# Kernel optimization log

Hardware: AMD Instinct MI355X
Metric: run time of the kernel (lower is better)

Reference implementation:

```python
import jax, jax.numpy as jnp
import numpy as np

D_MODEL, D_HID, N_EXPERTS, TOP_K = 1024, 4096, 8, 2

def setup_inputs() -> dict:
    key = jax.random.key(0)
    ks = jax.random.split(key, 6)
    B, T = 2, 2048
    x = jax.random.normal(ks[0], (B, T, D_MODEL), dtype=jnp.float32)
    gate_w = jax.random.normal(ks[1], (N_EXPERTS, D_MODEL), dtype=jnp.float32) * (1.0 / np.sqrt(D_MODEL))
    # kaiming_uniform-ish init for expert weights
    lim1 = np.sqrt(6.0 / D_MODEL)
    lim2 = np.sqrt(6.0 / D_HID)
    w1 = jax.random.uniform(ks[2], (N_EXPERTS, D_MODEL, D_HID), dtype=jnp.float32, minval=-lim1, maxval=lim1)
    w2 = jax.random.uniform(ks[3], (N_EXPERTS, D_HID, D_MODEL), dtype=jnp.float32, minval=-lim2, maxval=lim2)
    b1 = jnp.zeros((N_EXPERTS, 1, D_HID), dtype=jnp.float32)
    b2 = jnp.zeros((N_EXPERTS, 1, D_MODEL), dtype=jnp.float32)
    return {"x": x, "gate_w": gate_w, "w1": w1, "b1": b1, "w2": w2, "b2": b2}

def reference(x, gate_w, w1, b1, w2, b2):
    B, T, D = x.shape
    E = gate_w.shape[0]
    xf = x.reshape(-1, D)                              # [N, D]
    N = xf.shape[0]
    # Router: logits -> softmax -> top-k -> renormalize
    logits = jnp.einsum('nd,ed->ne', xf, gate_w)       # [N, E]
    scores = jax.nn.softmax(logits, axis=-1)
    top_w, top_i = jax.lax.top_k(scores, TOP_K)        # [N, K]
    top_w = top_w / jnp.sum(top_w, axis=-1, keepdims=True)
    # Dense combine weights (zero for unselected experts) — same math as
    # the padded-bmm dispatch/combine: padded slots have weight 0.
    gates = jnp.zeros((N, E), xf.dtype).at[jnp.arange(N)[:, None], top_i].add(top_w)  # [N, E]
    # Grouped expert MLP (computed densely; weighted combine zeroes unrouted experts)
    h = jax.nn.gelu(jnp.einsum('nd,edh->enh', xf, w1) + b1, approximate=False)  # [E, N, H]
    expert_out = jnp.einsum('enh,ehd->end', h, w2) + b2                          # [E, N, D]
    out = jnp.einsum('end,ne->nd', expert_out, gates)                            # [N, D]
    return out.reshape(B, T, D)
```

## Files before the change

### kernel.cpp

```cpp
#include <hip/hip_runtime.h>
#include <math.h>

#define NTOK 4096
#define DM   1024
#define DH   4096
#define NE   8
#define NSLOT (NTOK*2)
#define TMAX 72

typedef unsigned short u16;
typedef __attribute__((ext_vector_type(8))) short shortx8;
typedef __attribute__((ext_vector_type(4))) float floatx4;
typedef __attribute__((ext_vector_type(4))) int   intx4;

__device__ __forceinline__ u16 f2bf(float f) {
  union { float f; unsigned u; } c; c.f = f;
  unsigned r = c.u + 0x7fffu + ((c.u >> 16) & 1u);
  return (u16)(r >> 16);
}

__device__ __forceinline__ void async_cp16(const u16* g, u16* l) {
  __builtin_amdgcn_global_load_lds(
      (const __attribute__((address_space(1))) void*)g,
      (__attribute__((address_space(3))) void*)l, 16, 0, 0);
}

__global__ void cvt_x_kernel(const float* __restrict__ x, u16* __restrict__ xb) {
  int i = (blockIdx.x * 256 + threadIdx.x) * 8;
  float4 v0 = *(const float4*)(x + i);
  float4 v1 = *(const float4*)(x + i + 4);
  u16 tmp[8] = {f2bf(v0.x), f2bf(v0.y), f2bf(v0.z), f2bf(v0.w),
                f2bf(v1.x), f2bf(v1.y), f2bf(v1.z), f2bf(v1.w)};
  *(intx4*)(xb + i) = *(intx4*)tmp;
}

template<int K, int NW>
__global__ __launch_bounds__(256) void transpose_kernel(const float* __restrict__ W,
                                                        u16* __restrict__ Wt) {
  __shared__ u16 tile[64][66];
  int e = blockIdx.z;
  int n0 = blockIdx.x * 64, k0 = blockIdx.y * 64;
  int tt = threadIdx.x;
  const float* src = W + (size_t)e * K * NW + (size_t)(k0 + (tt >> 2)) * NW + n0 + (tt & 3) * 16;
  int r = tt >> 2, c4 = (tt & 3) * 16;
  float4 v[4];
#pragma unroll
  for (int i = 0; i < 4; i++) v[i] = *(const float4*)(src + i * 4);
#pragma unroll
  for (int i = 0; i < 4; i++) {
    tile[r][c4 + 4 * i + 0] = f2bf(v[i].x);
    tile[r][c4 + 4 * i + 1] = f2bf(v[i].y);
    tile[r][c4 + 4 * i + 2] = f2bf(v[i].z);
    tile[r][c4 + 4 * i + 3] = f2bf(v[i].w);
  }
  __syncthreads();
  u16* dst = Wt + (size_t)e * NW * K + (size_t)n0 * K + k0;
#pragma unroll
  for (int p = 0; p < 2; p++) {
    int n = (tt >> 3) + p * 32;
    int kc = (tt & 7) * 8;
    u16 o[8];
#pragma unroll
    for (int i = 0; i < 8; i++) o[i] = tile[kc + i][n];
    *(intx4*)(dst + (size_t)n * K + kc) = *(intx4*)o;
  }
}

__global__ __launch_bounds__(256) void router_kernel(const float* __restrict__ x,
                                                     const float* __restrict__ gw,
                                                     int* __restrict__ eos,
                                                     float* __restrict__ wos) {
  int wave = threadIdx.x >> 6, lane = threadIdx.x & 63;
  int n = blockIdx.x * 4 + wave;
  const float* xr = x + (size_t)n * DM;
  float acc[NE];
#pragma unroll
  for (int e = 0; e < NE; e++) acc[e] = 0.f;
  for (int d = lane; d < DM; d += 64) {
    float xv = xr[d];
#pragma unroll
    for (int e = 0; e < NE; e++) acc[e] += xv * gw[e * DM + d];
  }
#pragma unroll
  for (int e = 0; e < NE; e++) {
    float v = acc[e];
#pragma unroll
    for (int off = 32; off > 0; off >>= 1) v += __shfl_xor(v, off, 64);
    acc[e] = v;
  }
  if (lane == 0) {
    int i0 = 0;
    for (int e = 1; e < NE; e++) if (acc[e] > acc[i0]) i0 = e;
    int i1 = (i0 == 0) ? 1 : 0;
    for (int e = 0; e < NE; e++) { if (e == i0) continue; if (acc[e] > acc[i1]) i1 = e; }
    float e1 = expf(acc[i1] - acc[i0]);
    float w0 = 1.f / (1.f + e1);
    eos[2 * n] = i0;  eos[2 * n + 1] = i1;
    wos[2 * n] = w0;  wos[2 * n + 1] = 1.f - w0;
  }
}

__global__ __launch_bounds__(256) void build_groups_kernel(
    const int* __restrict__ eos, const float* __restrict__ wos,
    int* __restrict__ goff, int* __restrict__ tok_of_g, float* __restrict__ w_of_g,
    int* __restrict__ tiles, int* __restrict__ ntiles) {
  __shared__ int pref[256][NE];
  __shared__ int tot[NE];
  __shared__ int ebase[NE + 1];
  int t = threadIdx.x;
  int c[NE];
#pragma unroll
  for (int e = 0; e < NE; e++) c[e] = 0;
  for (int i = 0; i < NSLOT / 256; i++) {
    int e = eos[t * (NSLOT / 256) + i];
#pragma unroll
    for (int q = 0; q < NE; q++) if (e == q) c[q]++;
  }
#pragma unroll
  for (int e = 0; e < NE; e++) pref[t][e] = c[e];
  __syncthreads();
  if (t < NE) {
    int run = 0;
    for (int i = 0; i < 256; i++) { int v = pref[i][t]; pref[i][t] = run; run += v; }
    tot[t] = run;
  }
  __syncthreads();
  if (t == 0) {
    int o = 0;
    for (int e = 0; e < NE; e++) { ebase[e] = o; o += tot[e]; }
    ebase[NE] = o;
    int nt = 0;
    for (int e = 0; e < NE; e++)
      for (int mb = 0; mb * 128 < tot[e]; mb++) tiles[nt++] = (e << 16) | mb;
    ntiles[0] = nt;
  }
  __syncthreads();
  int off[NE];
#pragma unroll
  for (int e = 0; e < NE; e++) off[e] = ebase[e] + pref[t][e];
  for (int i = 0; i < NSLOT / 256; i++) {
    int s = t * (NSLOT / 256) + i;
    int e = eos[s];
    int g = 0;
#pragma unroll
    for (int q = 0; q < NE; q++) if (e == q) { g = off[q]; off[q] = g + 1; }
    tok_of_g[g] = s >> 1;
    w_of_g[g] = wos[s];
  }
  if (t <= NE) goff[t] = ebase[t];
}

template<int K, int NOUT, int MODE, int KSPLIT>
__global__ __launch_bounds__(256) void moe_gemm(
    const u16* __restrict__ A, const u16* __restrict__ Wt, const float* __restrict__ bias,
    const int* __restrict__ goff, const int* __restrict__ tok_of_g,
    const float* __restrict__ w_of_g, const int* __restrict__ tiles,
    const int* __restrict__ ntiles,
    u16* __restrict__ Hout, float* __restrict__ Out) {
  const int KLEN = K / KSPLIT;
  const int NB = NOUT / 128;
  const int NWG = TMAX * NB * KSPLIT;
  int flat = blockIdx.x;
  int wgid = (flat & 7) * (NWG >> 3) + (flat >> 3);
  int nb   = wgid % NB;
  int rest = wgid / NB;
  int tl   = rest % TMAX;
  int kseg = rest / TMAX;
  if (tl >= ntiles[0]) return;
  int packed = tiles[tl];
  int e = packed >> 16;
  int mb = packed & 0xffff;
  int gb = goff[e];
  int cntE = goff[e + 1] - gb;
  int m0 = mb * 128;
  int mvalid = cntE - m0; if (mvalid > 128) mvalid = 128;
  int gbase = gb + m0;
  int n0 = nb * 128;
  int kbeg = kseg * KLEN;
  int tid = threadIdx.x;
  int lane = tid & 63, wave = tid >> 6;

  __shared__ __align__(16) u16 As[2][128 * 32];
  __shared__ __align__(16) u16 Bs[2][128 * 32];

  int sr = lane >> 2;
  int sc = (lane & 3) * 8;
  int scs = sc ^ (((sr >> 1) & 3) << 3);
  int ra0 = wave * 16 + sr;
  int ra1 = 64 + wave * 16 + sr;
  int ca0 = (ra0 < mvalid) ? ra0 : (mvalid - 1);
  int ca1 = (ra1 < mvalid) ? ra1 : (mvalid - 1);
  const u16 *pa0, *pa1;
  if (MODE == 0) {
    pa0 = A + (size_t)tok_of_g[gbase + ca0] * K + scs;
    pa1 = A + (size_t)tok_of_g[gbase + ca1] * K + scs;
  } else {
    pa0 = A + (size_t)(gbase + ca0) * K + scs;
    pa1 = A + (size_t)(gbase + ca1) * K + scs;
  }
  const u16* wte = Wt + (size_t)e * NOUT * K;
  const u16* pb0 = wte + (size_t)(n0 + ra0) * K + scs;
  const u16* pb1 = wte + (size_t)(n0 + ra1) * K + scs;

  int wm = wave >> 1, wn = wave & 1;
  int lr = lane & 15, lk = (lane >> 4) * 8;
  int lks = lk ^ (((lr >> 1) & 3) << 3);

  floatx4 acc[4][4];
#pragma unroll
  for (int i = 0; i < 4; i++)
#pragma unroll
    for (int j = 0; j < 4; j++) acc[i][j] = (floatx4){0.f, 0.f, 0.f, 0.f};

  auto stage = [&](int b, int k0) {
    async_cp16(pa0 + k0, &As[b][wave * 512]);
    async_cp16(pa1 + k0, &As[b][2048 + wave * 512]);
    async_cp16(pb0 + k0, &Bs[b][wave * 512]);
    async_cp16(pb1 + k0, &Bs[b][2048 + wave * 512]);
  };
  auto ldfrag = [&](int b, shortx8* af, shortx8* bfr) {
#pragma unroll
    for (int i = 0; i < 4; i++) {
      af[i]  = *(const shortx8*)&As[b][(wm * 64 + i * 16 + lr) * 32 + lks];
      bfr[i] = *(const shortx8*)&Bs[b][(wn * 64 + i * 16 + lr) * 32 + lks];
    }
  };
  auto domfma = [&](shortx8* af, shortx8* bfr) {
#pragma unroll
    for (int i = 0; i < 4; i++)
#pragma unroll
      for (int j = 0; j < 4; j++)
        acc[i][j] = __builtin_amdgcn_mfma_f32_16x16x32_bf16(af[i], bfr[j], acc[i][j], 0, 0, 0);
  };

  const int NT = KLEN / 32;
  stage(0, kbeg);
  stage(1, kbeg + 32);
  for (int t = 0; t < NT - 2; ++t) {
    int cur = t & 1;
    asm volatile("s_waitcnt vmcnt(4)" ::: "memory");
    __builtin_amdgcn_s_barrier();
    shortx8 af[4], bfr[4];
    ldfrag(cur, af, bfr);
    asm volatile("s_waitcnt lgkmcnt(0)" ::: "memory");
    __builtin_amdgcn_sched_barrier(0);
    __builtin_amdgcn_s_barrier();
    stage(cur, kbeg + (t + 2) * 32);
    domfma(af, bfr);
  }
  {
    asm volatile("s_waitcnt vmcnt(4)" ::: "memory");
    __builtin_amdgcn_s_barrier();
    shortx8 af[4], bfr[4];
    ldfrag(NT & 1, af, bfr);
    domfma(af, bfr);
  }
  {
    asm volatile("s_waitcnt vmcnt(0)" ::: "memory");
    __builtin_amdgcn_s_barrier();
    shortx8 af[4], bfr[4];
    ldfrag(1 - (NT & 1), af, bfr);
    domfma(af, bfr);
  }

  const float* bp = bias + (size_t)e * NOUT + n0;
  if (MODE == 0) {
#pragma unroll
    for (int i = 0; i < 4; i++) {
      int rowb = wm * 64 + i * 16 + (lane >> 4) * 4;
#pragma unroll
      for (int r = 0; r < 4; r++) {
        int grow = rowb + r;
        if (grow < mvalid) {
          size_t base = (size_t)(gbase + grow) * NOUT + n0;
#pragma unroll
          for (int j = 0; j < 4; j++) {
            int col = wn * 64 + j * 16 + lr;
            float v = acc[i][j][r] + bp[col];
            v = 0.5f * v * (1.f + erff(v * 0.70710678118654752f));
            Hout[base + col] = f2bf(v);
          }
        }
      }
    }
  } else {
#pragma unroll
    for (int i = 0; i < 4; i++) {
      int rowb = wm * 64 + i * 16 + (lane >> 4) * 4;
#pragma unroll
      for (int r = 0; r < 4; r++) {
        int grow = rowb + r;
        if (grow < mvalid) {
          int gi = gbase + grow;
          int t = tok_of_g[gi];
          float wg = w_of_g[gi];
          float* orow = Out + (size_t)t * DM + n0;
#pragma unroll
          for (int j = 0; j < 4; j++) {
            int col = wn * 64 + j * 16 + lr;
            float bb = (kseg == 0) ? bp[col] : 0.f;
            atomicAdd(&orow[col], wg * (acc[i][j][r] + bb));
          }
        }
      }
    }
  }
}

extern "C" void kernel_launch(void* const* d_in, const int* in_sizes, int n_in,
                              void* d_out, int out_size, void* d_ws, size_t ws_size,
                              hipStream_t stream) {
  const float* x  = (const float*)d_in[0];
  const float* gw = (const float*)d_in[1];
  const float* w1 = (const float*)d_in[2];
  const float* b1 = (const float*)d_in[3];
  const float* w2 = (const float*)d_in[4];
  const float* b2 = (const float*)d_in[5];
  float* out = (float*)d_out;
  char* ws = (char*)d_ws;

  u16* xb = (u16*)(ws + 0);
  u16* wt = (u16*)(ws + 8388608);
  u16* h  = (u16*)(ws + 75497472);
  char* meta = ws + 142606336;
  int*   eos      = (int*)(meta);
  int*   tok_of_g = (int*)(meta + 32768);
  float* wos      = (float*)(meta + 65536);
  float* w_of_g   = (float*)(meta + 98304);
  int*   goff     = (int*)(meta + 131072);
  int*   tiles    = (int*)(meta + 131200);
  int*   ntiles   = (int*)(meta + 131584);

  hipMemsetAsync(out, 0, (size_t)NTOK * DM * 4, stream);

  cvt_x_kernel<<<NTOK * DM / 8 / 256, 256, 0, stream>>>(x, xb);
  transpose_kernel<DM, DH><<<dim3(DH / 64, DM / 64, NE), 256, 0, stream>>>(w1, wt);
  router_kernel<<<NTOK / 4, 256, 0, stream>>>(x, gw, eos, wos);
  build_groups_kernel<<<1, 256, 0, stream>>>(eos, wos, goff, tok_of_g, w_of_g, tiles, ntiles);
  moe_gemm<DM, DH, 0, 1><<<TMAX * (DH / 128), 256, 0, stream>>>(
      xb, wt, b1, goff, tok_of_g, w_of_g, tiles, ntiles, h, nullptr);
  transpose_kernel<DH, DM><<<dim3(DM / 64, DH / 64, NE), 256, 0, stream>>>(w2, wt);
  moe_gemm<DH, DM, 1, 2><<<TMAX * (DM / 128) * 2, 256, 0, stream>>>(
      h, wt, b2, goff, tok_of_g, w_of_g, tiles, ntiles, nullptr, out);
}
```

Before: 757.5 us.

## Double K-tile depth to 64 with split fragment loads and priority-boosted MFMA

```diff
diff --git a/kernel.cpp b/kernel.cpp
--- a/kernel.cpp
+++ b/kernel.cpp
@@ -180,31 +180,25 @@
   int tid = threadIdx.x;
   int lane = tid & 63, wave = tid >> 6;
 
-  __shared__ __align__(16) u16 As[2][128 * 32];
-  __shared__ __align__(16) u16 Bs[2][128 * 32];
-
-  int sr = lane >> 2;
-  int sc = (lane & 3) * 8;
-  int scs = sc ^ (((sr >> 1) & 3) << 3);
-  int ra0 = wave * 16 + sr;
-  int ra1 = 64 + wave * 16 + sr;
-  int ca0 = (ra0 < mvalid) ? ra0 : (mvalid - 1);
-  int ca1 = (ra1 < mvalid) ? ra1 : (mvalid - 1);
-  const u16 *pa0, *pa1;
-  if (MODE == 0) {
-    pa0 = A + (size_t)tok_of_g[gbase + ca0] * K + scs;
-    pa1 = A + (size_t)tok_of_g[gbase + ca1] * K + scs;
-  } else {
-    pa0 = A + (size_t)(gbase + ca0) * K + scs;
-    pa1 = A + (size_t)(gbase + ca1) * K + scs;
-  }
+  __shared__ __align__(16) u16 As[2][128 * 64];
+  __shared__ __align__(16) u16 Bs[2][128 * 64];
+
+  int gcol = (((lane & 7) ^ (lane >> 3)) * 8);
+  const u16 *pA[4], *pB[4];
   const u16* wte = Wt + (size_t)e * NOUT * K;
-  const u16* pb0 = wte + (size_t)(n0 + ra0) * K + scs;
-  const u16* pb1 = wte + (size_t)(n0 + ra1) * K + scs;
+#pragma unroll
+  for (int i = 0; i < 4; i++) {
+    int rw = wave * 32 + i * 8 + (lane >> 3);
+    int cw = (rw < mvalid) ? rw : (mvalid - 1);
+    if (MODE == 0) pA[i] = A + (size_t)tok_of_g[gbase + cw] * K + gcol;
+    else           pA[i] = A + (size_t)(gbase + cw) * K + gcol;
+    pB[i] = wte + (size_t)(n0 + rw) * K + gcol;
+  }
 
   int wm = wave >> 1, wn = wave & 1;
-  int lr = lane & 15, lk = (lane >> 4) * 8;
-  int lks = lk ^ (((lr >> 1) & 3) << 3);
+  int lr = lane & 15;
+  int c0 = (((lane >> 4)) ^ (lr & 7)) * 8;
+  int c1 = ((4 + (lane >> 4)) ^ (lr & 7)) * 8;
 
   floatx4 acc[4][4];
 #pragma unroll
@@ -213,54 +207,75 @@
     for (int j = 0; j < 4; j++) acc[i][j] = (floatx4){0.f, 0.f, 0.f, 0.f};
 
   auto stage = [&](int b, int k0) {
-    async_cp16(pa0 + k0, &As[b][wave * 512]);
-    async_cp16(pa1 + k0, &As[b][2048 + wave * 512]);
-    async_cp16(pb0 + k0, &Bs[b][wave * 512]);
-    async_cp16(pb1 + k0, &Bs[b][2048 + wave * 512]);
+#pragma unroll
+    for (int i = 0; i < 4; i++)
+      async_cp16(pA[i] + k0, &As[b][(wave * 32 + i * 8) * 64]);
+#pragma unroll
+    for (int i = 0; i < 4; i++)
+      async_cp16(pB[i] + k0, &Bs[b][(wave * 32 + i * 8) * 64]);
   };
-  auto ldfrag = [&](int b, shortx8* af, shortx8* bfr) {
+
+  const int NT = KLEN / 64;
+  stage(0, kbeg);
+  stage(1, kbeg + 64);
+
+  shortx8 af[8], bfr[8];
+  auto ldfrag_half = [&](int b, int h) {
+    int cc = h ? c1 : c0;
 #pragma unroll
     for (int i = 0; i < 4; i++) {
-      af[i]  = *(const shortx8*)&As[b][(wm * 64 + i * 16 + lr) * 32 + lks];
-      bfr[i] = *(const shortx8*)&Bs[b][(wn * 64 + i * 16 + lr) * 32 + lks];
+      af[h * 4 + i]  = *(const shortx8*)&As[b][(wm * 64 + i * 16 + lr) * 64 + cc];
+      bfr[h * 4 + i] = *(const shortx8*)&Bs[b][(wn * 64 + i * 16 + lr) * 64 + cc];
     }
   };
-  auto domfma = [&](shortx8* af, shortx8* bfr) {
+  auto mfma_half = [&](int h) {
 #pragma unroll
     for (int i = 0; i < 4; i++)
 #pragma unroll
       for (int j = 0; j < 4; j++)
-        acc[i][j] = __builtin_amdgcn_mfma_f32_16x16x32_bf16(af[i], bfr[j], acc[i][j], 0, 0, 0);
+        acc[i][j] = __builtin_amdgcn_mfma_f32_16x16x32_bf16(af[h * 4 + i], bfr[h * 4 + j],
+                                                            acc[i][j], 0, 0, 0);
   };
 
-  const int NT = KLEN / 32;
-  stage(0, kbeg);
-  stage(1, kbeg + 32);
   for (int t = 0; t < NT - 2; ++t) {
     int cur = t & 1;
-    asm volatile("s_waitcnt vmcnt(4)" ::: "memory");
+    asm volatile("s_waitcnt vmcnt(8)" ::: "memory");
     __builtin_amdgcn_s_barrier();
-    shortx8 af[4], bfr[4];
-    ldfrag(cur, af, bfr);
+    asm volatile("" ::: "memory");
+    ldfrag_half(cur, 0);
+    asm volatile("" ::: "memory");
+    ldfrag_half(cur, 1);
+    asm volatile("s_waitcnt lgkmcnt(8)" ::: "memory");
+    __builtin_amdgcn_sched_barrier(0);
+    __builtin_amdgcn_s_setprio(1);
+    mfma_half(0);
+    __builtin_amdgcn_s_setprio(0);
     asm volatile("s_waitcnt lgkmcnt(0)" ::: "memory");
     __builtin_amdgcn_sched_barrier(0);
     __builtin_amdgcn_s_barrier();
-    stage(cur, kbeg + (t + 2) * 32);
-    domfma(af, bfr);
-  }
-  {
-    asm volatile("s_waitcnt vmcnt(4)" ::: "memory");
+    __builtin_amdgcn_sched_barrier(0);
+    stage(cur, kbeg + (t + 2) * 64);
+    __builtin_amdgcn_sched_barrier(0);
+    __builtin_amdgcn_s_setprio(1);
+    mfma_half(1);
+    __builtin_amdgcn_s_setprio(0);
+  }
+#pragma unroll
+  for (int tt2 = 0; tt2 < 2; ++tt2) {
+    int cur = (NT + tt2) & 1;
+    if (tt2 == 0) asm volatile("s_waitcnt vmcnt(8)" ::: "memory");
+    else          asm volatile("s_waitcnt vmcnt(0)" ::: "memory");
     __builtin_amdgcn_s_barrier();
-    shortx8 af[4], bfr[4];
-    ldfrag(NT & 1, af, bfr);
-    domfma(af, bfr);
-  }
-  {
-    asm volatile("s_waitcnt vmcnt(0)" ::: "memory");
-    __builtin_amdgcn_s_barrier();
-    shortx8 af[4], bfr[4];
-    ldfrag(1 - (NT & 1), af, bfr);
-    domfma(af, bfr);
+    asm volatile("" ::: "memory");
+    ldfrag_half(cur, 0);
+    asm volatile("" ::: "memory");
+    ldfrag_half(cur, 1);
+    asm volatile("s_waitcnt lgkmcnt(8)" ::: "memory");
+    __builtin_amdgcn_sched_barrier(0);
+    mfma_half(0);
+    asm volatile("s_waitcnt lgkmcnt(0)" ::: "memory");
+    __builtin_amdgcn_sched_barrier(0);
+    mfma_half(1);
   }
 
   const float* bp = bias + (size_t)e * NOUT + n0;
```

After: 714.7 us. -5.7%, faster.
